# Kernel tuning notes

Hardware: AMD Instinct MI355X
Metric: run time of the kernel (lower is better)

Reference implementation:

```python
import jax, jax.numpy as jnp
import numpy as np

N_WIRES = 6
DIM = 1 << N_WIRES  # 64, equals input channel dim C for amplitude encoding
HID = N_WIRES       # hidden_dim = len(ops)


def _rx(theta):
    c = jnp.cos(theta / 2).astype(jnp.complex64)
    s = jnp.sin(theta / 2).astype(jnp.complex64)
    return jnp.stack([jnp.stack([c, -1j * s]), jnp.stack([-1j * s, c])])


def _ry(theta):
    c = jnp.cos(theta / 2).astype(jnp.complex64)
    s = jnp.sin(theta / 2).astype(jnp.complex64)
    return jnp.stack([jnp.stack([c, -s]), jnp.stack([s, c])])


def _apply_1q(state, U, wire):
    # state: (N, 2, 2, ..., 2); apply 2x2 U on qubit axis wire+1
    s = jnp.moveaxis(state, wire + 1, 1)
    s = jnp.einsum('ab,nb...->na...', U, s)
    return jnp.moveaxis(s, 1, wire + 1)


def _apply_cnot(state, c, t):
    # flip target axis where control bit == 1
    s = jnp.moveaxis(state, (c + 1, t + 1), (1, 2))
    s = jnp.concatenate([s[:, :1], jnp.flip(s[:, 1:2], axis=2)], axis=1)
    return jnp.moveaxis(s, (1, 2), (c + 1, t + 1))


def _expval_z(state, wire):
    # <Z_wire> = P(bit=0) - P(bit=1)
    p = state.real ** 2 + state.imag ** 2
    p = jnp.moveaxis(p, wire + 1, 1).reshape(p.shape[0], 2, -1)
    return p[:, 0].sum(-1) - p[:, 1].sum(-1)


def _value_layer(x_flat, params, qk):
    # amplitude encoding: normalize input into state amplitudes (C == DIM)
    norm = jnp.linalg.norm(x_flat, axis=-1, keepdims=True)
    psi = (x_flat / norm).astype(jnp.complex64)
    state = psi.reshape((x_flat.shape[0],) + (2,) * N_WIRES)
    rx0, ry0, ry1 = params[0], params[1], params[2]
    for j in range(N_WIRES):
        state = _apply_1q(state, _rx(rx0[j]), j)
        state = _apply_1q(state, _ry(ry0[j]), j)
    for j in range(N_WIRES):
        state = _apply_cnot(state, j, (j + 1) % N_WIRES)
    for j in range(N_WIRES):
        state = _apply_1q(state, _ry(ry1[j]), j)
    if qk:
        z0 = _expval_z(state, 0)
        return jnp.stack([z0] * HID, axis=-1)  # qk=True replicates wire-0 <Z>
    return jnp.stack([_expval_z(state, w) for w in range(N_WIRES)], axis=-1)


def setup_inputs() -> dict:
    key = jax.random.key(0)
    k1, k2, k3, k4 = jax.random.split(key, 4)
    B, T, C = 16, 2048, DIM
    return {
        'x': jax.random.normal(k1, (B, T, C), dtype=jnp.float32),
        'params_q': jax.random.normal(k2, (3, N_WIRES), dtype=jnp.float32),
        'params_k': jax.random.normal(k3, (3, N_WIRES), dtype=jnp.float32),
        'params_v': jax.random.normal(k4, (3, N_WIRES), dtype=jnp.float32),
    }


def reference(x, params_q, params_k, params_v):
    B, T, C = x.shape
    xf = x.reshape(B * T, C)
    q = _value_layer(xf, params_q, True).reshape(B, T, HID)
    k = _value_layer(xf, params_k, True).reshape(B, T, HID)
    v = _value_layer(xf, params_v, False).reshape(B, T, HID)
    scores = jnp.einsum('btd,bsd->bts', q, k) / jnp.sqrt(jnp.float32(HID))
    attn = jax.nn.softmax(scores, axis=-1)
    return jnp.einsum('bts,bsd->btd', attn, v)
```

## Files before the change

kernel.cpp:

```cpp
#include <hip/hip_runtime.h>
#include <math.h>

#define NWIRES 6
#define DIM 64
#define NTOK 32768
#define NBATCH 16
#define TPB 2048
#define NMOM 16
#define SQRT6F 2.4494897427831781f

__global__ void qsa_prep(const float* __restrict__ pq,
                         const float* __restrict__ pk,
                         const float* __restrict__ pv,
                         float* __restrict__ cs) {
    int i = threadIdx.x;
    if (i >= 54) return;
    int circ = i / 18, g = i % 18;
    const float* p = (circ == 0) ? pq : (circ == 1 ? pk : pv);
    float s, c;
    sincosf(0.5f * p[g], &s, &c);
    cs[i * 2 + 0] = c;
    cs[i * 2 + 1] = s;
}

template<int M>
__device__ __forceinline__ void rx_g(float* re, float* im, float c, float s) {
#pragma unroll
    for (int i = 0; i < DIM; ++i) {
        if (i & M) continue;
        int j = i | M;
        float r0 = re[i], i0 = im[i], r1 = re[j], i1 = im[j];
        re[i] = c * r0 + s * i1;
        im[i] = c * i0 - s * r1;
        re[j] = c * r1 + s * i0;
        im[j] = c * i1 - s * r0;
    }
}

template<int M>
__device__ __forceinline__ void ry_g(float* re, float* im, float c, float s) {
#pragma unroll
    for (int i = 0; i < DIM; ++i) {
        if (i & M) continue;
        int j = i | M;
        float r0 = re[i], i0 = im[i], r1 = re[j], i1 = im[j];
        re[i] = c * r0 - s * r1;
        im[i] = c * i0 - s * i1;
        re[j] = c * r1 + s * r0;
        im[j] = c * i1 + s * i0;
    }
}

template<int MC, int MT>
__device__ __forceinline__ void cnot_g(float* re, float* im) {
#pragma unroll
    for (int i = 0; i < DIM; ++i) {
        if (!(i & MC) || (i & MT)) continue;
        int j = i | MT;
        float tr = re[i]; re[i] = re[j]; re[j] = tr;
        float ti = im[i]; im[i] = im[j]; im[j] = ti;
    }
}

__global__ __attribute__((amdgpu_waves_per_eu(2, 2)))
__launch_bounds__(64) void qsa_sim(
        const float* __restrict__ x,
        const float* __restrict__ cs,
        float* __restrict__ zq,
        float* __restrict__ kv) {
    int token = blockIdx.x * 64 + threadIdx.x;
    int circ = blockIdx.y;
    const float* P = cs + circ * 36;

    float re[DIM], im[DIM];
    const float4* xp4 = (const float4*)(x + (size_t)token * DIM);
#pragma unroll
    for (int k = 0; k < DIM / 4; ++k) {
        float4 v = xp4[k];
        re[4*k+0] = v.x; re[4*k+1] = v.y; re[4*k+2] = v.z; re[4*k+3] = v.w;
        im[4*k+0] = 0.f; im[4*k+1] = 0.f; im[4*k+2] = 0.f; im[4*k+3] = 0.f;
    }

    rx_g<32>(re, im, P[0],  P[1]);  ry_g<32>(re, im, P[12], P[13]);
    rx_g<16>(re, im, P[2],  P[3]);  ry_g<16>(re, im, P[14], P[15]);
    rx_g< 8>(re, im, P[4],  P[5]);  ry_g< 8>(re, im, P[16], P[17]);
    rx_g< 4>(re, im, P[6],  P[7]);  ry_g< 4>(re, im, P[18], P[19]);
    rx_g< 2>(re, im, P[8],  P[9]);  ry_g< 2>(re, im, P[20], P[21]);
    rx_g< 1>(re, im, P[10], P[11]); ry_g< 1>(re, im, P[22], P[23]);
    cnot_g<32,16>(re, im);
    cnot_g<16, 8>(re, im);
    cnot_g< 8, 4>(re, im);
    cnot_g< 4, 2>(re, im);
    cnot_g< 2, 1>(re, im);
    cnot_g< 1,32>(re, im);
    ry_g<32>(re, im, P[24], P[25]);
    ry_g<16>(re, im, P[26], P[27]);
    ry_g< 8>(re, im, P[28], P[29]);
    ry_g< 4>(re, im, P[30], P[31]);
    ry_g< 2>(re, im, P[32], P[33]);
    ry_g< 1>(re, im, P[34], P[35]);

    float norm2 = 0.f, s0=0.f, s1=0.f, s2=0.f, s3=0.f, s4=0.f, s5=0.f;
#pragma unroll
    for (int i = 0; i < DIM; ++i) {
        float p = re[i]*re[i] + im[i]*im[i];
        norm2 += p;
        if (!(i & 32)) s0 += p;
        if (!(i & 16)) s1 += p;
        if (!(i &  8)) s2 += p;
        if (!(i &  4)) s3 += p;
        if (!(i &  2)) s4 += p;
        if (!(i &  1)) s5 += p;
    }
    float inv = 1.0f / norm2;
    if (circ == 0) {
        zq[token] = SQRT6F * (2.f*s0 - norm2) * inv;
    } else if (circ == 1) {
        kv[(size_t)token * 8 + 0] = (2.f*s0 - norm2) * inv;
    } else {
        float* o = kv + (size_t)token * 8;
        o[1] = (2.f*s0 - norm2) * inv;
        o[2] = (2.f*s1 - norm2) * inv;
        o[3] = (2.f*s2 - norm2) * inv;
        o[4] = (2.f*s3 - norm2) * inv;
        o[5] = (2.f*s4 - norm2) * inv;
        o[6] = (2.f*s5 - norm2) * inv;
        o[7] = 0.f;
    }
}

__global__ __attribute__((amdgpu_waves_per_eu(1, 2)))
__launch_bounds__(64) void qsa_moments_partial(
        const float* __restrict__ kv,
        float* __restrict__ mpart) {
    int blk = blockIdx.x;
    int b = blk >> 3, c = blk & 7;
    int lane = threadIdx.x;
    float S[NMOM], H[NMOM][6];
#pragma unroll
    for (int m = 0; m < NMOM; ++m) {
        S[m] = 0.f;
#pragma unroll
        for (int w = 0; w < 6; ++w) H[m][w] = 0.f;
    }
    const float* base = kv + ((size_t)(b * TPB + c * 256)) * 8;
#pragma unroll
    for (int r = 0; r < 4; ++r) {
        const float4* e = (const float4*)(base + (size_t)(r * 64 + lane) * 8);
        float4 e0 = e[0], e1 = e[1];
        float z = e0.x;
        float v0 = e0.y, v1 = e0.z, v2 = e0.w, v3 = e1.x, v4 = e1.y, v5 = e1.z;
        float p = 1.f;
#pragma unroll
        for (int m = 0; m < NMOM; ++m) {
            S[m] += p;
            H[m][0] += p * v0; H[m][1] += p * v1; H[m][2] += p * v2;
            H[m][3] += p * v3; H[m][4] += p * v4; H[m][5] += p * v5;
            p *= z;
        }
    }
#pragma unroll
    for (int d = 32; d >= 1; d >>= 1) {
#pragma unroll
        for (int m = 0; m < NMOM; ++m) {
            S[m] += __shfl_xor(S[m], d, 64);
#pragma unroll
            for (int w = 0; w < 6; ++w) H[m][w] += __shfl_xor(H[m][w], d, 64);
        }
    }
    if (lane == 0) {
        float* o = mpart + (size_t)blk * 112;
#pragma unroll
        for (int m = 0; m < NMOM; ++m) {
            float* om = o + m * 7;
            om[0] = S[m];
            om[1] = H[m][0]; om[2] = H[m][1]; om[3] = H[m][2];
            om[4] = H[m][3]; om[5] = H[m][4]; om[6] = H[m][5];
        }
    }
}

__global__ void qsa_moments_combine(const float* __restrict__ mpart,
                                    float* __restrict__ mom) {
#pragma unroll
    for (int it = 0; it < 7; ++it) {
        int i = it * 256 + threadIdx.x;
        int b = i / 112, j = i % 112;
        float s = 0.f;
#pragma unroll
        for (int c = 0; c < 8; ++c) s += mpart[(size_t)(b * 8 + c) * 112 + j];
        mom[(size_t)b * 112 + j] = s;
    }
}

__global__ __launch_bounds__(256) void qsa_eval(
        const float* __restrict__ zq,
        const float* __restrict__ mom,
        float* __restrict__ out) {
    int t = blockIdx.x * 256 + threadIdx.x;
    int b = t >> 11;
    const float* M = mom + (size_t)b * 112;
    float a = zq[t];
    float den = 0.f, o0 = 0.f, o1 = 0.f, o2 = 0.f, o3 = 0.f, o4 = 0.f, o5 = 0.f;
    float p = 1.f;
#pragma unroll
    for (int m = 0; m < NMOM; ++m) {
        const float* mm = M + m * 7;
        den += p * mm[0];
        o0 += p * mm[1]; o1 += p * mm[2]; o2 += p * mm[3];
        o3 += p * mm[4]; o4 += p * mm[5]; o5 += p * mm[6];
        p *= a * (1.0f / (m + 1));
    }
    float inv = 1.0f / den;
    float* o = out + (size_t)t * 6;
    float2* o2p = (float2*)o;
    o2p[0] = make_float2(o0 * inv, o1 * inv);
    o2p[1] = make_float2(o2 * inv, o3 * inv);
    o2p[2] = make_float2(o4 * inv, o5 * inv);
}

extern "C" void kernel_launch(void* const* d_in, const int* in_sizes, int n_in,
                              void* d_out, int out_size, void* d_ws, size_t ws_size,
                              hipStream_t stream) {
    const float* x  = (const float*)d_in[0];
    const float* pq = (const float*)d_in[1];
    const float* pk = (const float*)d_in[2];
    const float* pv = (const float*)d_in[3];
    float* w = (float*)d_ws;
    float* cs    = w;
    float* zq    = w + 128;
    float* kv    = w + 128 + NTOK;
    float* mpart = w + 128 + NTOK + NTOK * 8;
    float* mom   = mpart + 128 * 112;
    float* out   = (float*)d_out;

    qsa_prep<<<1, 64, 0, stream>>>(pq, pk, pv, cs);
    qsa_sim<<<dim3(NTOK / 64, 3), 64, 0, stream>>>(x, cs, zq, kv);
    qsa_moments_partial<<<NBATCH * 8, 64, 0, stream>>>(kv, mpart);
    qsa_moments_combine<<<1, 256, 0, stream>>>(mpart, mom);
    qsa_eval<<<NTOK / 256, 256, 0, stream>>>(zq, mom, out);
}
```

Measured before the change: 99.82 us.

## Split each token's 64-amplitude state across two lanes with shuffle exchange

```diff
diff --git a/kernel.cpp b/kernel.cpp
--- a/kernel.cpp
+++ b/kernel.cpp
@@ -23,10 +23,12 @@
     cs[i * 2 + 1] = s;
 }
 
+__device__ __forceinline__ float pswap(float v) { return __shfl_xor(v, 1, 64); }
+
 template<int M>
-__device__ __forceinline__ void rx_g(float* re, float* im, float c, float s) {
-#pragma unroll
-    for (int i = 0; i < DIM; ++i) {
+__device__ __forceinline__ void rx_l(float* re, float* im, float c, float s) {
+#pragma unroll
+    for (int i = 0; i < 32; ++i) {
         if (i & M) continue;
         int j = i | M;
         float r0 = re[i], i0 = im[i], r1 = re[j], i1 = im[j];
@@ -38,9 +40,9 @@
 }
 
 template<int M>
-__device__ __forceinline__ void ry_g(float* re, float* im, float c, float s) {
-#pragma unroll
-    for (int i = 0; i < DIM; ++i) {
+__device__ __forceinline__ void ry_l(float* re, float* im, float c, float s) {
+#pragma unroll
+    for (int i = 0; i < 32; ++i) {
         if (i & M) continue;
         int j = i | M;
         float r0 = re[i], i0 = im[i], r1 = re[j], i1 = im[j];
@@ -52,9 +54,9 @@
 }
 
 template<int MC, int MT>
-__device__ __forceinline__ void cnot_g(float* re, float* im) {
-#pragma unroll
-    for (int i = 0; i < DIM; ++i) {
+__device__ __forceinline__ void cnot_l(float* re, float* im) {
+#pragma unroll
+    for (int i = 0; i < 32; ++i) {
         if (!(i & MC) || (i & MT)) continue;
         int j = i | MT;
         float tr = re[i]; re[i] = re[j]; re[j] = tr;
@@ -62,70 +64,125 @@
     }
 }
 
-__global__ __attribute__((amdgpu_waves_per_eu(2, 2)))
+__device__ __forceinline__ void rx_s(float* re, float* im, float c, float s) {
+#pragma unroll
+    for (int i = 0; i < 32; ++i) {
+        float pre = pswap(re[i]), pim = pswap(im[i]);
+        re[i] = c * re[i] + s * pim;
+        im[i] = c * im[i] - s * pre;
+    }
+}
+
+__device__ __forceinline__ void ry_s(float* re, float* im, float c, float ss) {
+#pragma unroll
+    for (int i = 0; i < 32; ++i) {
+        float pre = pswap(re[i]), pim = pswap(im[i]);
+        re[i] = c * re[i] + ss * pre;
+        im[i] = c * im[i] + ss * pim;
+    }
+}
+
+__device__ __forceinline__ void cnot_c01(float* re, float* im, int p) {
+#pragma unroll
+    for (int i = 0; i < 32; ++i) {
+        if (i & 16) continue;
+        int j = i | 16;
+        float r0 = re[i], r1 = re[j], i0 = im[i], i1 = im[j];
+        re[i] = p ? r1 : r0;  re[j] = p ? r0 : r1;
+        im[i] = p ? i1 : i0;  im[j] = p ? i0 : i1;
+    }
+}
+
+__device__ __forceinline__ void cnot_c50(float* re, float* im) {
+#pragma unroll
+    for (int i = 1; i < 32; i += 2) {
+        re[i] = pswap(re[i]);
+        im[i] = pswap(im[i]);
+    }
+}
+
+__global__ __attribute__((amdgpu_waves_per_eu(4, 8)))
 __launch_bounds__(64) void qsa_sim(
         const float* __restrict__ x,
         const float* __restrict__ cs,
         float* __restrict__ zq,
         float* __restrict__ kv) {
-    int token = blockIdx.x * 64 + threadIdx.x;
+    int g = blockIdx.x * 64 + threadIdx.x;
+    int p = g & 1;
+    int token = g >> 1;
     int circ = blockIdx.y;
     const float* P = cs + circ * 36;
 
-    float re[DIM], im[DIM];
-    const float4* xp4 = (const float4*)(x + (size_t)token * DIM);
-#pragma unroll
-    for (int k = 0; k < DIM / 4; ++k) {
+    float re[32], im[32];
+    const float4* xp4 = (const float4*)(x + (size_t)g * 32);
+#pragma unroll
+    for (int k = 0; k < 8; ++k) {
         float4 v = xp4[k];
         re[4*k+0] = v.x; re[4*k+1] = v.y; re[4*k+2] = v.z; re[4*k+3] = v.w;
         im[4*k+0] = 0.f; im[4*k+1] = 0.f; im[4*k+2] = 0.f; im[4*k+3] = 0.f;
     }
-
-    rx_g<32>(re, im, P[0],  P[1]);  ry_g<32>(re, im, P[12], P[13]);
-    rx_g<16>(re, im, P[2],  P[3]);  ry_g<16>(re, im, P[14], P[15]);
-    rx_g< 8>(re, im, P[4],  P[5]);  ry_g< 8>(re, im, P[16], P[17]);
-    rx_g< 4>(re, im, P[6],  P[7]);  ry_g< 4>(re, im, P[18], P[19]);
-    rx_g< 2>(re, im, P[8],  P[9]);  ry_g< 2>(re, im, P[20], P[21]);
-    rx_g< 1>(re, im, P[10], P[11]); ry_g< 1>(re, im, P[22], P[23]);
-    cnot_g<32,16>(re, im);
-    cnot_g<16, 8>(re, im);
-    cnot_g< 8, 4>(re, im);
-    cnot_g< 4, 2>(re, im);
-    cnot_g< 2, 1>(re, im);
-    cnot_g< 1,32>(re, im);
-    ry_g<32>(re, im, P[24], P[25]);
-    ry_g<16>(re, im, P[26], P[27]);
-    ry_g< 8>(re, im, P[28], P[29]);
-    ry_g< 4>(re, im, P[30], P[31]);
-    ry_g< 2>(re, im, P[32], P[33]);
-    ry_g< 1>(re, im, P[34], P[35]);
-
-    float norm2 = 0.f, s0=0.f, s1=0.f, s2=0.f, s3=0.f, s4=0.f, s5=0.f;
-#pragma unroll
-    for (int i = 0; i < DIM; ++i) {
-        float p = re[i]*re[i] + im[i]*im[i];
-        norm2 += p;
-        if (!(i & 32)) s0 += p;
-        if (!(i & 16)) s1 += p;
-        if (!(i &  8)) s2 += p;
-        if (!(i &  4)) s3 += p;
-        if (!(i &  2)) s4 += p;
-        if (!(i &  1)) s5 += p;
-    }
+    float sgn = p ? 1.f : -1.f;
+
+    rx_s(re, im, P[0], P[1]);
+    rx_l<16>(re, im, P[2],  P[3]);
+    rx_l< 8>(re, im, P[4],  P[5]);
+    rx_l< 4>(re, im, P[6],  P[7]);
+    rx_l< 2>(re, im, P[8],  P[9]);
+    rx_l< 1>(re, im, P[10], P[11]);
+    ry_s(re, im, P[12], sgn * P[13]);
+    ry_l<16>(re, im, P[14], P[15]);
+    ry_l< 8>(re, im, P[16], P[17]);
+    ry_l< 4>(re, im, P[18], P[19]);
+    ry_l< 2>(re, im, P[20], P[21]);
+    ry_l< 1>(re, im, P[22], P[23]);
+    cnot_c01(re, im, p);
+    cnot_l<16, 8>(re, im);
+    cnot_l< 8, 4>(re, im);
+    cnot_l< 4, 2>(re, im);
+    cnot_l< 2, 1>(re, im);
+    cnot_c50(re, im);
+    ry_s(re, im, P[24], sgn * P[25]);
+    ry_l<16>(re, im, P[26], P[27]);
+    ry_l< 8>(re, im, P[28], P[29]);
+    ry_l< 4>(re, im, P[30], P[31]);
+    ry_l< 2>(re, im, P[32], P[33]);
+    ry_l< 1>(re, im, P[34], P[35]);
+
+    float nl = 0.f, t1=0.f, t2=0.f, t3=0.f, t4=0.f, t5=0.f;
+#pragma unroll
+    for (int i = 0; i < 32; ++i) {
+        float pi = re[i]*re[i] + im[i]*im[i];
+        nl += pi;
+        if (!(i & 16)) t1 += pi;
+        if (!(i &  8)) t2 += pi;
+        if (!(i &  4)) t3 += pi;
+        if (!(i &  2)) t4 += pi;
+        if (!(i &  1)) t5 += pi;
+    }
+    float np = pswap(nl);
+    float norm2 = nl + np;
+    float S0 = p ? np : nl;
     float inv = 1.0f / norm2;
+    float z0 = (2.f * S0 - norm2) * inv;
+
     if (circ == 0) {
-        zq[token] = SQRT6F * (2.f*s0 - norm2) * inv;
+        if (p == 0) zq[token] = SQRT6F * z0;
     } else if (circ == 1) {
-        kv[(size_t)token * 8 + 0] = (2.f*s0 - norm2) * inv;
+        if (p == 0) kv[(size_t)token * 8] = z0;
     } else {
+        float S1 = t1 + pswap(t1);
+        float S2 = t2 + pswap(t2);
+        float S3 = t3 + pswap(t3);
+        float S4 = t4 + pswap(t4);
+        float S5 = t5 + pswap(t5);
+        float z1 = (2.f*S1 - norm2) * inv;
+        float z2 = (2.f*S2 - norm2) * inv;
+        float z3 = (2.f*S3 - norm2) * inv;
+        float z4 = (2.f*S4 - norm2) * inv;
+        float z5 = (2.f*S5 - norm2) * inv;
         float* o = kv + (size_t)token * 8;
-        o[1] = (2.f*s0 - norm2) * inv;
-        o[2] = (2.f*s1 - norm2) * inv;
-        o[3] = (2.f*s2 - norm2) * inv;
-        o[4] = (2.f*s3 - norm2) * inv;
-        o[5] = (2.f*s4 - norm2) * inv;
-        o[6] = (2.f*s5 - norm2) * inv;
-        o[7] = 0.f;
+        if (p == 0) { o[1] = z0; o[2] = z1; o[3] = z2; }
+        else        { o[4] = z3; o[5] = z4; o[6] = z5; }
     }
 }
 
@@ -150,13 +207,13 @@
         float4 e0 = e[0], e1 = e[1];
         float z = e0.x;
         float v0 = e0.y, v1 = e0.z, v2 = e0.w, v3 = e1.x, v4 = e1.y, v5 = e1.z;
-        float p = 1.f;
+        float pw = 1.f;
 #pragma unroll
         for (int m = 0; m < NMOM; ++m) {
-            S[m] += p;
-            H[m][0] += p * v0; H[m][1] += p * v1; H[m][2] += p * v2;
-            H[m][3] += p * v3; H[m][4] += p * v4; H[m][5] += p * v5;
-            p *= z;
+            S[m] += pw;
+            H[m][0] += pw * v0; H[m][1] += pw * v1; H[m][2] += pw * v2;
+            H[m][3] += pw * v3; H[m][4] += pw * v4; H[m][5] += pw * v5;
+            pw *= z;
         }
     }
 #pragma unroll
@@ -202,14 +259,14 @@
     const float* M = mom + (size_t)b * 112;
     float a = zq[t];
     float den = 0.f, o0 = 0.f, o1 = 0.f, o2 = 0.f, o3 = 0.f, o4 = 0.f, o5 = 0.f;
-    float p = 1.f;
+    float pw = 1.f;
 #pragma unroll
     for (int m = 0; m < NMOM; ++m) {
         const float* mm = M + m * 7;
-        den += p * mm[0];
-        o0 += p * mm[1]; o1 += p * mm[2]; o2 += p * mm[3];
-        o3 += p * mm[4]; o4 += p * mm[5]; o5 += p * mm[6];
-        p *= a * (1.0f / (m + 1));
+        den += pw * mm[0];
+        o0 += pw * mm[1]; o1 += pw * mm[2]; o2 += pw * mm[3];
+        o3 += pw * mm[4]; o4 += pw * mm[5]; o5 += pw * mm[6];
+        pw *= a * (1.0f / (m + 1));
     }
     float inv = 1.0f / den;
     float* o = out + (size_t)t * 6;
@@ -235,7 +292,7 @@
     float* out   = (float*)d_out;
 
     qsa_prep<<<1, 64, 0, stream>>>(pq, pk, pv, cs);
-    qsa_sim<<<dim3(NTOK / 64, 3), 64, 0, stream>>>(x, cs, zq, kv);
+    qsa_sim<<<dim3(NTOK * 2 / 64, 3), 64, 0, stream>>>(x, cs, zq, kv);
     qsa_moments_partial<<<NBATCH * 8, 64, 0, stream>>>(kv, mpart);
     qsa_moments_combine<<<1, 256, 0, stream>>>(mpart, mom);
     qsa_eval<<<NTOK / 256, 256, 0, stream>>>(zq, mom, out);
```

Result: faster. 96.89 us (-2.9%).

## Fold RX layer into Walsh-Hadamard diagonal and split complex state across thread pairs

Applied to the files above, without the earlier changes.

```diff
diff --git a/kernel.cpp b/kernel.cpp
--- a/kernel.cpp
+++ b/kernel.cpp
@@ -8,124 +8,162 @@
 #define TPB 2048
 #define NMOM 16
 #define SQRT6F 2.4494897427831781f
+#define CSTRIDE 160
 
 __global__ void qsa_prep(const float* __restrict__ pq,
                          const float* __restrict__ pk,
                          const float* __restrict__ pv,
                          float* __restrict__ cs) {
-    int i = threadIdx.x;
-    if (i >= 54) return;
-    int circ = i / 18, g = i % 18;
-    const float* p = (circ == 0) ? pq : (circ == 1 ? pk : pv);
-    float s, c;
-    sincosf(0.5f * p[g], &s, &c);
-    cs[i * 2 + 0] = c;
-    cs[i * 2 + 1] = s;
+    int b = threadIdx.x;
+    for (int circ = 0; circ < 3; ++circ) {
+        const float* p = (circ == 0) ? pq : (circ == 1 ? pk : pv);
+        float* T = cs + circ * CSTRIDE;
+        float d = 0.f;
+#pragma unroll
+        for (int j = 0; j < 6; ++j)
+            d += 0.5f * p[j] * ((b & (32 >> j)) ? -1.f : 1.f);
+        float sd, cd;
+        sincosf(d, &sd, &cd);
+        T[b] = cd;
+        T[64 + b] = sd;
+        if (b < 12) {
+            float s, c;
+            sincosf(0.5f * p[6 + b], &s, &c);
+            T[128 + b * 2 + 0] = c;
+            T[128 + b * 2 + 1] = s;
+        }
+    }
 }
 
 template<int M>
-__device__ __forceinline__ void rx_g(float* re, float* im, float c, float s) {
+__device__ __forceinline__ void whad(float* v) {
 #pragma unroll
     for (int i = 0; i < DIM; ++i) {
         if (i & M) continue;
         int j = i | M;
-        float r0 = re[i], i0 = im[i], r1 = re[j], i1 = im[j];
-        re[i] = c * r0 + s * i1;
-        im[i] = c * i0 - s * r1;
-        re[j] = c * r1 + s * i0;
-        im[j] = c * i1 - s * r0;
+        float a = v[i], b = v[j];
+        v[i] = a + b;
+        v[j] = a - b;
     }
 }
 
 template<int M>
-__device__ __forceinline__ void ry_g(float* re, float* im, float c, float s) {
+__device__ __forceinline__ void ryr(float* v, float c, float s) {
 #pragma unroll
     for (int i = 0; i < DIM; ++i) {
         if (i & M) continue;
         int j = i | M;
-        float r0 = re[i], i0 = im[i], r1 = re[j], i1 = im[j];
-        re[i] = c * r0 - s * r1;
-        im[i] = c * i0 - s * i1;
-        re[j] = c * r1 + s * r0;
-        im[j] = c * i1 + s * i0;
+        float a = v[i], b = v[j];
+        v[i] = c * a - s * b;
+        v[j] = s * a + c * b;
     }
 }
 
 template<int MC, int MT>
-__device__ __forceinline__ void cnot_g(float* re, float* im) {
+__device__ __forceinline__ void cnr(float* v) {
 #pragma unroll
     for (int i = 0; i < DIM; ++i) {
         if (!(i & MC) || (i & MT)) continue;
         int j = i | MT;
-        float tr = re[i]; re[i] = re[j]; re[j] = tr;
-        float ti = im[i]; im[i] = im[j]; im[j] = ti;
-    }
-}
-
-__global__ __attribute__((amdgpu_waves_per_eu(2, 2)))
-__launch_bounds__(64) void qsa_sim(
+        float t = v[i]; v[i] = v[j]; v[j] = t;
+    }
+}
+
+__global__ __attribute__((amdgpu_waves_per_eu(1, 4)))
+__launch_bounds__(256) void qsa_sim(
         const float* __restrict__ x,
         const float* __restrict__ cs,
         float* __restrict__ zq,
         float* __restrict__ kv) {
-    int token = blockIdx.x * 64 + threadIdx.x;
+    int g = blockIdx.x * 256 + threadIdx.x;
+    int par = g & 1;
+    int token = g >> 1;
     int circ = blockIdx.y;
-    const float* P = cs + circ * 36;
-
-    float re[DIM], im[DIM];
+    const float* T = cs + circ * CSTRIDE;
+    const float* P = T + 128;
+
+    float v[DIM];
     const float4* xp4 = (const float4*)(x + (size_t)token * DIM);
 #pragma unroll
     for (int k = 0; k < DIM / 4; ++k) {
-        float4 v = xp4[k];
-        re[4*k+0] = v.x; re[4*k+1] = v.y; re[4*k+2] = v.z; re[4*k+3] = v.w;
-        im[4*k+0] = 0.f; im[4*k+1] = 0.f; im[4*k+2] = 0.f; im[4*k+3] = 0.f;
-    }
-
-    rx_g<32>(re, im, P[0],  P[1]);  ry_g<32>(re, im, P[12], P[13]);
-    rx_g<16>(re, im, P[2],  P[3]);  ry_g<16>(re, im, P[14], P[15]);
-    rx_g< 8>(re, im, P[4],  P[5]);  ry_g< 8>(re, im, P[16], P[17]);
-    rx_g< 4>(re, im, P[6],  P[7]);  ry_g< 4>(re, im, P[18], P[19]);
-    rx_g< 2>(re, im, P[8],  P[9]);  ry_g< 2>(re, im, P[20], P[21]);
-    rx_g< 1>(re, im, P[10], P[11]); ry_g< 1>(re, im, P[22], P[23]);
-    cnot_g<32,16>(re, im);
-    cnot_g<16, 8>(re, im);
-    cnot_g< 8, 4>(re, im);
-    cnot_g< 4, 2>(re, im);
-    cnot_g< 2, 1>(re, im);
-    cnot_g< 1,32>(re, im);
-    ry_g<32>(re, im, P[24], P[25]);
-    ry_g<16>(re, im, P[26], P[27]);
-    ry_g< 8>(re, im, P[28], P[29]);
-    ry_g< 4>(re, im, P[30], P[31]);
-    ry_g< 2>(re, im, P[32], P[33]);
-    ry_g< 1>(re, im, P[34], P[35]);
-
-    float norm2 = 0.f, s0=0.f, s1=0.f, s2=0.f, s3=0.f, s4=0.f, s5=0.f;
-#pragma unroll
-    for (int i = 0; i < DIM; ++i) {
-        float p = re[i]*re[i] + im[i]*im[i];
-        norm2 += p;
-        if (!(i & 32)) s0 += p;
-        if (!(i & 16)) s1 += p;
-        if (!(i &  8)) s2 += p;
-        if (!(i &  4)) s3 += p;
-        if (!(i &  2)) s4 += p;
-        if (!(i &  1)) s5 += p;
-    }
-    float inv = 1.0f / norm2;
-    if (circ == 0) {
-        zq[token] = SQRT6F * (2.f*s0 - norm2) * inv;
-    } else if (circ == 1) {
-        kv[(size_t)token * 8 + 0] = (2.f*s0 - norm2) * inv;
+        float4 q = xp4[k];
+        v[4*k+0] = q.x; v[4*k+1] = q.y; v[4*k+2] = q.z; v[4*k+3] = q.w;
+    }
+
+    whad<32>(v); whad<16>(v); whad<8>(v); whad<4>(v); whad<2>(v); whad<1>(v);
+    const float4* tp4 = (const float4*)(T + par * 64);
+#pragma unroll
+    for (int k = 0; k < DIM / 4; ++k) {
+        float4 q = tp4[k];
+        v[4*k+0] *= q.x; v[4*k+1] *= q.y; v[4*k+2] *= q.z; v[4*k+3] *= q.w;
+    }
+    whad<32>(v); whad<16>(v); whad<8>(v); whad<4>(v); whad<2>(v); whad<1>(v);
+
+    ryr<32>(v, P[0],  P[1]);
+    ryr<16>(v, P[2],  P[3]);
+    ryr< 8>(v, P[4],  P[5]);
+    ryr< 4>(v, P[6],  P[7]);
+    ryr< 2>(v, P[8],  P[9]);
+    ryr< 1>(v, P[10], P[11]);
+    cnr<32,16>(v);
+    cnr<16, 8>(v);
+    cnr< 8, 4>(v);
+    cnr< 4, 2>(v);
+    cnr< 2, 1>(v);
+    cnr< 1,32>(v);
+    ryr<32>(v, P[12], P[13]);
+    ryr<16>(v, P[14], P[15]);
+    ryr< 8>(v, P[16], P[17]);
+    ryr< 4>(v, P[18], P[19]);
+    ryr< 2>(v, P[20], P[21]);
+    ryr< 1>(v, P[22], P[23]);
+
+    if (circ < 2) {
+        float nl = 0.f, s0 = 0.f;
+#pragma unroll
+        for (int i = 0; i < DIM; ++i) {
+            float p2 = v[i] * v[i];
+            nl += p2;
+            if (!(i & 32)) s0 += p2;
+        }
+        float norm2 = nl + __shfl_xor(nl, 1, 64);
+        float S0 = s0 + __shfl_xor(s0, 1, 64);
+        float z0 = (2.f * S0 - norm2) / norm2;
+        if (par == 0) {
+            if (circ == 0) zq[token] = SQRT6F * z0;
+            else           kv[(size_t)token * 8] = z0;
+        }
     } else {
+        float nl = 0.f, s0=0.f, s1=0.f, s2=0.f, s3=0.f, s4=0.f, s5=0.f;
+#pragma unroll
+        for (int i = 0; i < DIM; ++i) {
+            float p2 = v[i] * v[i];
+            nl += p2;
+            if (!(i & 32)) s0 += p2;
+            if (!(i & 16)) s1 += p2;
+            if (!(i &  8)) s2 += p2;
+            if (!(i &  4)) s3 += p2;
+            if (!(i &  2)) s4 += p2;
+            if (!(i &  1)) s5 += p2;
+        }
+        float norm2 = nl + __shfl_xor(nl, 1, 64);
+        float S0 = s0 + __shfl_xor(s0, 1, 64);
+        float S1 = s1 + __shfl_xor(s1, 1, 64);
+        float S2 = s2 + __shfl_xor(s2, 1, 64);
+        float S3 = s3 + __shfl_xor(s3, 1, 64);
+        float S4 = s4 + __shfl_xor(s4, 1, 64);
+        float S5 = s5 + __shfl_xor(s5, 1, 64);
+        float inv = 1.0f / norm2;
         float* o = kv + (size_t)token * 8;
-        o[1] = (2.f*s0 - norm2) * inv;
-        o[2] = (2.f*s1 - norm2) * inv;
-        o[3] = (2.f*s2 - norm2) * inv;
-        o[4] = (2.f*s3 - norm2) * inv;
-        o[5] = (2.f*s4 - norm2) * inv;
-        o[6] = (2.f*s5 - norm2) * inv;
-        o[7] = 0.f;
+        if (par == 0) {
+            o[1] = (2.f*S0 - norm2) * inv;
+            o[2] = (2.f*S1 - norm2) * inv;
+            o[3] = (2.f*S2 - norm2) * inv;
+        } else {
+            o[4] = (2.f*S3 - norm2) * inv;
+            o[5] = (2.f*S4 - norm2) * inv;
+            o[6] = (2.f*S5 - norm2) * inv;
+        }
     }
 }
 
@@ -150,13 +188,13 @@
         float4 e0 = e[0], e1 = e[1];
         float z = e0.x;
         float v0 = e0.y, v1 = e0.z, v2 = e0.w, v3 = e1.x, v4 = e1.y, v5 = e1.z;
-        float p = 1.f;
+        float pw = 1.f;
 #pragma unroll
         for (int m = 0; m < NMOM; ++m) {
-            S[m] += p;
-            H[m][0] += p * v0; H[m][1] += p * v1; H[m][2] += p * v2;
-            H[m][3] += p * v3; H[m][4] += p * v4; H[m][5] += p * v5;
-            p *= z;
+            S[m] += pw;
+            H[m][0] += pw * v0; H[m][1] += pw * v1; H[m][2] += pw * v2;
+            H[m][3] += pw * v3; H[m][4] += pw * v4; H[m][5] += pw * v5;
+            pw *= z;
         }
     }
 #pragma unroll
@@ -180,36 +218,33 @@
     }
 }
 
-__global__ void qsa_moments_combine(const float* __restrict__ mpart,
-                                    float* __restrict__ mom) {
-#pragma unroll
-    for (int it = 0; it < 7; ++it) {
-        int i = it * 256 + threadIdx.x;
-        int b = i / 112, j = i % 112;
-        float s = 0.f;
-#pragma unroll
-        for (int c = 0; c < 8; ++c) s += mpart[(size_t)(b * 8 + c) * 112 + j];
-        mom[(size_t)b * 112 + j] = s;
-    }
-}
-
 __global__ __launch_bounds__(256) void qsa_eval(
         const float* __restrict__ zq,
-        const float* __restrict__ mom,
+        const float* __restrict__ mpart,
         float* __restrict__ out) {
-    int t = blockIdx.x * 256 + threadIdx.x;
-    int b = t >> 11;
-    const float* M = mom + (size_t)b * 112;
+    __shared__ float sm[112];
+    int bk = blockIdx.x;
+    int b = bk >> 3;
+    int tid = threadIdx.x;
+    if (tid < 112) {
+        float s = 0.f;
+#pragma unroll
+        for (int c = 0; c < 8; ++c) s += mpart[(size_t)(b * 8 + c) * 112 + tid];
+        sm[tid] = s;
+    }
+    __syncthreads();
+
+    int t = bk * 256 + tid;
     float a = zq[t];
     float den = 0.f, o0 = 0.f, o1 = 0.f, o2 = 0.f, o3 = 0.f, o4 = 0.f, o5 = 0.f;
-    float p = 1.f;
+    float pw = 1.f;
 #pragma unroll
     for (int m = 0; m < NMOM; ++m) {
-        const float* mm = M + m * 7;
-        den += p * mm[0];
-        o0 += p * mm[1]; o1 += p * mm[2]; o2 += p * mm[3];
-        o3 += p * mm[4]; o4 += p * mm[5]; o5 += p * mm[6];
-        p *= a * (1.0f / (m + 1));
+        const float* mm = sm + m * 7;
+        den += pw * mm[0];
+        o0 += pw * mm[1]; o1 += pw * mm[2]; o2 += pw * mm[3];
+        o3 += pw * mm[4]; o4 += pw * mm[5]; o5 += pw * mm[6];
+        pw *= a * (1.0f / (m + 1));
     }
     float inv = 1.0f / den;
     float* o = out + (size_t)t * 6;
@@ -228,15 +263,13 @@
     const float* pv = (const float*)d_in[3];
     float* w = (float*)d_ws;
     float* cs    = w;
-    float* zq    = w + 128;
-    float* kv    = w + 128 + NTOK;
-    float* mpart = w + 128 + NTOK + NTOK * 8;
-    float* mom   = mpart + 128 * 112;
+    float* zq    = w + 512;
+    float* kv    = w + 512 + NTOK;
+    float* mpart = w + 512 + NTOK + NTOK * 8;
     float* out   = (float*)d_out;
 
     qsa_prep<<<1, 64, 0, stream>>>(pq, pk, pv, cs);
-    qsa_sim<<<dim3(NTOK / 64, 3), 64, 0, stream>>>(x, cs, zq, kv);
+    qsa_sim<<<dim3(NTOK * 2 / 256, 3), 256, 0, stream>>>(x, cs, zq, kv);
     qsa_moments_partial<<<NBATCH * 8, 64, 0, stream>>>(kv, mpart);
-    qsa_moments_combine<<<1, 256, 0, stream>>>(mpart, mom);
-    qsa_eval<<<NTOK / 256, 256, 0, stream>>>(zq, mom, out);
-}
+    qsa_eval<<<NTOK / 256, 256, 0, stream>>>(zq, mpart, out);
+}
```

After: 90.72 us. 1.1x faster.
